# Kernel tuning notes

Measured on AMD Instinct MI355X. Metric: run time of the kernel, lower is better.

The kernel has to match this reference:

```python
import jax, jax.numpy as jnp
import numpy as np

B, H, W, C = 64, 56, 56, 128
WIN, SHIFT, NH = 7, 3, 4
HD = C // NH
N = WIN * WIN
nWh, nWw = H // WIN, W // WIN
nW = nWh * nWw
MLP_H = 4 * C


def _rel_pos_index():
    # same construction as WindowAttention.__init__
    coords = np.stack(np.meshgrid(np.arange(WIN), np.arange(WIN), indexing='ij')).reshape(2, -1)
    rel = coords[:, :, None] - coords[:, None, :]
    rel = rel.transpose(1, 2, 0).copy()
    rel[..., 0] += WIN - 1
    rel[..., 1] += WIN - 1
    rel[..., 0] *= 2 * WIN - 1
    return rel.sum(-1)  # (N, N) int


def _attn_mask():
    # standard SW-MSA mask (0 / -100 like the torch reference)
    img = np.zeros((H, W))
    cnt = 0
    for hs in (slice(0, -WIN), slice(-WIN, -SHIFT), slice(-SHIFT, None)):
        for ws in (slice(0, -WIN), slice(-WIN, -SHIFT), slice(-SHIFT, None)):
            img[hs, ws] = cnt
            cnt += 1
    m = img.reshape(nWh, WIN, nWw, WIN).transpose(0, 2, 1, 3).reshape(nW, N)
    diff = m[:, None, :] - m[:, :, None]
    return np.where(diff != 0, -100.0, 0.0).astype(np.float32)  # (nW, N, N)


def _ln(x, g, b):
    mu = x.mean(-1, keepdims=True)
    var = ((x - mu) ** 2).mean(-1, keepdims=True)
    return (x - mu) / jnp.sqrt(var + 1e-5) * g + b


def setup_inputs() -> dict:
    key = jax.random.key(0)
    ks = jax.random.split(key, 6)
    s = 0.02
    return {
        'x': jax.random.normal(ks[0], (B, H * W, C), jnp.float32),
        'ln1_g': jnp.ones((C,), jnp.float32),
        'ln1_b': jnp.zeros((C,), jnp.float32),
        'qkv_w': jax.random.normal(ks[1], (3 * C, C), jnp.float32) * s,
        'qkv_b': jnp.zeros((3 * C,), jnp.float32),
        'rpb_table': jax.random.normal(ks[2], ((2 * WIN - 1) ** 2, NH), jnp.float32) * s,
        'proj_w': jax.random.normal(ks[3], (C, C), jnp.float32) * s,
        'proj_b': jnp.zeros((C,), jnp.float32),
        'ln2_g': jnp.ones((C,), jnp.float32),
        'ln2_b': jnp.zeros((C,), jnp.float32),
        'fc1_w': jax.random.normal(ks[4], (MLP_H, C), jnp.float32) * s,
        'fc1_b': jnp.zeros((MLP_H,), jnp.float32),
        'fc2_w': jax.random.normal(ks[5], (C, MLP_H), jnp.float32) * s,
        'fc2_b': jnp.zeros((C,), jnp.float32),
    }


def reference(x, ln1_g, ln1_b, qkv_w, qkv_b, rpb_table, proj_w, proj_b,
              ln2_g, ln2_b, fc1_w, fc1_b, fc2_w, fc2_b):
    rpi = jnp.asarray(_rel_pos_index())          # (N, N)
    mask = jnp.asarray(_attn_mask())             # (nW, N, N)

    shortcut = x
    h = _ln(x, ln1_g, ln1_b).reshape(B, H, W, C)
    # cyclic shift
    h = jnp.roll(h, (-SHIFT, -SHIFT), axis=(1, 2))
    # window partition -> (B*nW, N, C)
    wins = h.reshape(B, nWh, WIN, nWw, WIN, C).transpose(0, 1, 3, 2, 4, 5).reshape(B * nW, N, C)

    # window attention
    qkv = (wins @ qkv_w.T + qkv_b).reshape(B * nW, N, 3, NH, HD).transpose(2, 0, 3, 1, 4)
    q, k, v = qkv[0] * (HD ** -0.5), qkv[1], qkv[2]   # (B*nW, NH, N, HD)
    attn = jnp.einsum('bhnd,bhmd->bhnm', q, k)
    bias = rpb_table[rpi.reshape(-1)].reshape(N, N, NH).transpose(2, 0, 1)  # (NH, N, N)
    attn = attn + bias[None]
    attn = attn.reshape(B, nW, NH, N, N) + mask[None, :, None]
    attn = jax.nn.softmax(attn.reshape(B * nW, NH, N, N), axis=-1)
    o = jnp.einsum('bhnm,bhmd->bhnd', attn, v).transpose(0, 2, 1, 3).reshape(B * nW, N, C)
    o = o @ proj_w.T + proj_b

    # window reverse + reverse shift
    o = o.reshape(B, nWh, nWw, WIN, WIN, C).transpose(0, 1, 3, 2, 4, 5).reshape(B, H, W, C)
    o = jnp.roll(o, (SHIFT, SHIFT), axis=(1, 2)).reshape(B, H * W, C)

    x = shortcut + o
    # MLP residual (exact GELU, as nn.GELU default)
    h2 = _ln(x, ln2_g, ln2_b)
    h2 = jax.nn.gelu(h2 @ fc1_w.T + fc1_b, approximate=False) @ fc2_w.T + fc2_b
    return x + h2
```

## Files before the change

kernel.cpp:

```cpp
#include <hip/hip_runtime.h>
#include <math.h>

#define B_  64
#define Cc  128
#define L_  3136

typedef __bf16 b8v __attribute__((ext_vector_type(8)));
typedef __bf16 b4v __attribute__((ext_vector_type(4)));
typedef float  f4v __attribute__((ext_vector_type(4)));

__device__ __forceinline__ f4v mfma16(b8v a, b8v b, f4v c) {
    return __builtin_amdgcn_mfma_f32_16x16x32_bf16(a, b, c, 0, 0, 0);
}
__device__ __forceinline__ int region(int h, int w) {
    int a = (h < 49) ? 0 : ((h < 53) ? 1 : 2);
    int b = (w < 49) ? 0 : ((w < 53) ? 1 : 2);
    return a * 3 + b;
}

__global__ __launch_bounds__(256) void prep_kernel(
    const float* __restrict__ qkv_w, const float* __restrict__ proj_w,
    const float* __restrict__ fc1_w, const float* __restrict__ fc2_w,
    const float* __restrict__ rpb,
    __bf16* __restrict__ wsb, float* __restrict__ bm)
{
    int i = blockIdx.x * 256 + threadIdx.x;
    if      (i <  49152) wsb[i] = (__bf16)qkv_w[i];
    else if (i <  65536) wsb[i] = (__bf16)proj_w[i - 49152];
    else if (i < 131072) wsb[i] = (__bf16)fc1_w[i - 65536];
    else if (i < 196608) wsb[i] = (__bf16)fc2_w[i - 131072];
    else {
        int idx = i - 196608;
        int jj = idx & 63, ii = (idx >> 6) & 63, h = (idx >> 12) & 3, wt = idx >> 14;
        float v;
        if (jj >= 49)      v = -1e30f;
        else if (ii >= 49) v = 0.f;
        else {
            int ih = ii / 7, iw = ii - ih * 7, jh = jj / 7, jw = jj - jh * 7;
            v = rpb[((ih - jh + 6) * 13 + (iw - jw + 6)) * 4 + h];
            int WH = (wt & 2) ? 49 : 0, WW = (wt & 1) ? 49 : 0;
            if (region(WH + ih, WW + iw) != region(WH + jh, WW + jw)) v -= 100.f;
        }
        bm[idx] = v;
    }
}

__global__ __launch_bounds__(256, 2) void swin_kernel(
    const float* __restrict__ x,
    const float* __restrict__ g1, const float* __restrict__ b1,
    const float* __restrict__ qkv_b, const float* __restrict__ proj_b,
    const __bf16* __restrict__ wqkv, const __bf16* __restrict__ wproj,
    const float* __restrict__ bm,
    float* __restrict__ out)
{
    __shared__ __bf16 a_s[64 * 136];
    __shared__ __bf16 Q_s[64 * 136];
    __shared__ __bf16 K_s[64 * 136];
    __shared__ __bf16 VT_s[128 * 72];

    const int tid = threadIdx.x, w = tid >> 6, lane = tid & 63;
    const int quad = lane >> 4, r16 = lane & 15;
    const int blk = blockIdx.x, b = blk >> 6, wi = blk & 63;
    const int wh = wi >> 3, ww = wi & 7;
    const int wt = ((wh == 7) ? 2 : 0) | ((ww == 7) ? 1 : 0);
    const float scale = 0.17677669529663687f;

    {
        f4v gg0 = *(const f4v*)(g1 + r16 * 8), gg1 = *(const f4v*)(g1 + r16 * 8 + 4);
        f4v bb0 = *(const f4v*)(b1 + r16 * 8), bb1 = *(const f4v*)(b1 + r16 * 8 + 4);
        #pragma unroll
        for (int it = 0; it < 4; it++) {
            int local = it * 4 + quad;
            int t = w * 16 + local;
            b8v o;
            #pragma unroll
            for (int e = 0; e < 8; e++) o[e] = (__bf16)0.f;
            if (t < 49) {
                int th = t / 7, tw = t - th * 7;
                int sh = wh * 7 + th + 3; if (sh >= 56) sh -= 56;
                int sw = ww * 7 + tw + 3; if (sw >= 56) sw -= 56;
                const float* xp = x + (b * L_ + sh * 56 + sw) * Cc + r16 * 8;
                f4v x0 = *(const f4v*)(xp), x1 = *(const f4v*)(xp + 4);
                float s = 0.f, q = 0.f;
                #pragma unroll
                for (int e = 0; e < 4; e++) {
                    s += x0[e] + x1[e];
                    q += x0[e] * x0[e] + x1[e] * x1[e];
                }
                s += __shfl_xor(s, 1, 64); q += __shfl_xor(q, 1, 64);
                s += __shfl_xor(s, 2, 64); q += __shfl_xor(q, 2, 64);
                s += __shfl_xor(s, 4, 64); q += __shfl_xor(q, 4, 64);
                s += __shfl_xor(s, 8, 64); q += __shfl_xor(q, 8, 64);
                float mu = s * (1.f / 128.f);
                float rs = rsqrtf(q * (1.f / 128.f) - mu * mu + 1e-5f);
                #pragma unroll
                for (int e = 0; e < 4; e++) {
                    o[e]     = (__bf16)((x0[e] - mu) * rs * gg0[e] + bb0[e]);
                    o[4 + e] = (__bf16)((x1[e] - mu) * rs * gg1[e] + bb1[e]);
                }
            }
            *(b8v*)(a_s + local * 136 + w * 16 * 136 + r16 * 8) = o;
        }
    }
    __syncthreads();

    {
        b8v A[4][4];
        #pragma unroll
        for (int mt = 0; mt < 4; mt++)
            #pragma unroll
            for (int i = 0; i < 4; i++)
                A[mt][i] = *(const b8v*)(a_s + (mt * 16 + r16) * 136 + i * 32 + quad * 8);

        #pragma unroll
        for (int nt6 = 0; nt6 < 6; nt6++) {
            const int col = w * 96 + nt6 * 16;
            const __bf16* bp = wqkv + (col + r16) * 128 + quad * 8;
            b8v B0 = *(const b8v*)(bp),      B1 = *(const b8v*)(bp + 32);
            b8v B2 = *(const b8v*)(bp + 64), B3 = *(const b8v*)(bp + 96);
            float bias = qkv_b[col + r16];
            #pragma unroll
            for (int mt = 0; mt < 4; mt++) {
                f4v acc = {0.f, 0.f, 0.f, 0.f};
                acc = mfma16(A[mt][0], B0, acc);
                acc = mfma16(A[mt][1], B1, acc);
                acc = mfma16(A[mt][2], B2, acc);
                acc = mfma16(A[mt][3], B3, acc);
                if (col < 128) {
                    #pragma unroll
                    for (int r = 0; r < 4; r++)
                        Q_s[(mt * 16 + quad * 4 + r) * 136 + col + r16] =
                            (__bf16)((acc[r] + bias) * scale);
                } else if (col < 256) {
                    #pragma unroll
                    for (int r = 0; r < 4; r++)
                        K_s[(mt * 16 + quad * 4 + r) * 136 + col - 128 + r16] =
                            (__bf16)(acc[r] + bias);
                } else {
                    b4v pk;
                    #pragma unroll
                    for (int r = 0; r < 4; r++) pk[r] = (__bf16)(acc[r] + bias);
                    *(b4v*)(VT_s + (col - 256 + r16) * 72 + mt * 16 + quad * 4) = pk;
                }
            }
        }
    }
    __syncthreads();

    f4v o_acc[4][2];
    #pragma unroll
    for (int h = 0; h < 4; h++)
        #pragma unroll
        for (int n = 0; n < 2; n++)
            o_acc[h][n] = (f4v){0.f, 0.f, 0.f, 0.f};

    const float* bmw = bm + wt * 4 * 4096;
    __bf16* scr = a_s + w * 16 * 136;

    #pragma unroll
    for (int h = 0; h < 4; h++) {
        b8v qf = *(const b8v*)(Q_s + (w * 16 + r16) * 136 + h * 32 + quad * 8);
        f4v s[4];
        #pragma unroll
        for (int nt = 0; nt < 4; nt++) {
            b8v kf = *(const b8v*)(K_s + (nt * 16 + r16) * 136 + h * 32 + quad * 8);
            f4v z = {0.f, 0.f, 0.f, 0.f};
            s[nt] = mfma16(qf, kf, z);
        }
        const float* bmp = bmw + h * 4096 + (w * 16 + quad * 4) * 64 + r16;
        #pragma unroll
        for (int nt = 0; nt < 4; nt++)
            #pragma unroll
            for (int r = 0; r < 4; r++)
                s[nt][r] += bmp[r * 64 + nt * 16];
        {
            float mx[4], sm[4];
            #pragma unroll
            for (int r = 0; r < 4; r++)
                mx[r] = fmaxf(fmaxf(s[0][r], s[1][r]), fmaxf(s[2][r], s[3][r]));
            #pragma unroll
            for (int mk = 1; mk < 16; mk <<= 1)
                #pragma unroll
                for (int r = 0; r < 4; r++)
                    mx[r] = fmaxf(mx[r], __shfl_xor(mx[r], mk, 64));
            #pragma unroll
            for (int r = 0; r < 4; r++) {
                s[0][r] = expf(s[0][r] - mx[r]);
                s[1][r] = expf(s[1][r] - mx[r]);
                s[2][r] = expf(s[2][r] - mx[r]);
                s[3][r] = expf(s[3][r] - mx[r]);
                sm[r] = s[0][r] + s[1][r] + s[2][r] + s[3][r];
            }
            #pragma unroll
            for (int mk = 1; mk < 16; mk <<= 1)
                #pragma unroll
                for (int r = 0; r < 4; r++)
                    sm[r] += __shfl_xor(sm[r], mk, 64);
            #pragma unroll
            for (int r = 0; r < 4; r++) {
                float inv = 1.f / sm[r];
                s[0][r] *= inv; s[1][r] *= inv; s[2][r] *= inv; s[3][r] *= inv;
            }
        }
        #pragma unroll
        for (int nt = 0; nt < 4; nt++)
            #pragma unroll
            for (int r = 0; r < 4; r++)
                scr[(quad * 4 + r) * 136 + nt * 16 + r16] = (__bf16)s[nt][r];
        #pragma unroll
        for (int ks = 0; ks < 2; ks++) {
            b8v pf = *(const b8v*)(scr + r16 * 136 + ks * 32 + quad * 8);
            #pragma unroll
            for (int nt = 0; nt < 2; nt++) {
                b8v vf = *(const b8v*)(VT_s + (h * 32 + nt * 16 + r16) * 72 + ks * 32 + quad * 8);
                o_acc[h][nt] = mfma16(pf, vf, o_acc[h][nt]);
            }
        }
    }

    #pragma unroll
    for (int h = 0; h < 4; h++)
        #pragma unroll
        for (int nt = 0; nt < 2; nt++)
            #pragma unroll
            for (int r = 0; r < 4; r++)
                scr[(quad * 4 + r) * 136 + h * 32 + nt * 16 + r16] = (__bf16)o_acc[h][nt][r];
    __syncthreads();

    {
        b8v O[4][4];
        #pragma unroll
        for (int mt = 0; mt < 4; mt++)
            #pragma unroll
            for (int i = 0; i < 4; i++)
                O[mt][i] = *(const b8v*)(a_s + (mt * 16 + r16) * 136 + i * 32 + quad * 8);

        #pragma unroll
        for (int nt = 0; nt < 2; nt++) {
            const int col = w * 32 + nt * 16;
            const __bf16* bp = wproj + (col + r16) * 128 + quad * 8;
            b8v B0 = *(const b8v*)(bp),      B1 = *(const b8v*)(bp + 32);
            b8v B2 = *(const b8v*)(bp + 64), B3 = *(const b8v*)(bp + 96);
            float pb = proj_b[col + r16];
            #pragma unroll
            for (int mt = 0; mt < 4; mt++) {
                f4v acc = {0.f, 0.f, 0.f, 0.f};
                acc = mfma16(O[mt][0], B0, acc);
                acc = mfma16(O[mt][1], B1, acc);
                acc = mfma16(O[mt][2], B2, acc);
                acc = mfma16(O[mt][3], B3, acc);
                #pragma unroll
                for (int r = 0; r < 4; r++) {
                    int t = mt * 16 + quad * 4 + r;
                    if (t < 49) {
                        int th = t / 7, tw = t - th * 7;
                        int sh = wh * 7 + th + 3; if (sh >= 56) sh -= 56;
                        int sw = ww * 7 + tw + 3; if (sw >= 56) sw -= 56;
                        int off = (b * L_ + sh * 56 + sw) * Cc + col + r16;
                        out[off] = x[off] + acc[r] + pb;
                    }
                }
            }
        }
    }
}

__global__ __launch_bounds__(256, 2) void mlp_kernel(
    float* __restrict__ out,
    const float* __restrict__ g2, const float* __restrict__ b2,
    const __bf16* __restrict__ wfc1, const __bf16* __restrict__ wfc2,
    const float* __restrict__ fc1_b, const float* __restrict__ fc2_b)
{
    __shared__ __align__(16) char u_s[69632];
    __bf16* x2 = (__bf16*)u_s;
    __bf16* h1 = (__bf16*)(u_s + 34816);
    float*  o_s = (float*)u_s;

    const int tid = threadIdx.x, w = tid >> 6, lane = tid & 63;
    const int quad = lane >> 4, r16 = lane & 15;
    const int rowbase = blockIdx.x * 128;

    #pragma unroll
    for (int p = 0; p < 2; p++) {
        const int r = p * 64 + (tid >> 2), sub = tid & 3;
        const float* xp = out + (rowbase + r) * Cc + sub * 32;
        f4v xa[8];
        #pragma unroll
        for (int j = 0; j < 8; j++) xa[j] = *(const f4v*)(xp + j * 4);
        float s = 0.f, q = 0.f;
        #pragma unroll
        for (int j = 0; j < 8; j++)
            #pragma unroll
            for (int e = 0; e < 4; e++) { float v = xa[j][e]; s += v; q += v * v; }
        s += __shfl_xor(s, 1, 64); q += __shfl_xor(q, 1, 64);
        s += __shfl_xor(s, 2, 64); q += __shfl_xor(q, 2, 64);
        float mu = s * (1.f / 128.f);
        float rs = rsqrtf(q * (1.f / 128.f) - mu * mu + 1e-5f);
        #pragma unroll
        for (int j = 0; j < 8; j += 2) {
            int c = sub * 32 + j * 4;
            f4v gg0 = *(const f4v*)(g2 + c), gg1 = *(const f4v*)(g2 + c + 4);
            f4v bb0 = *(const f4v*)(b2 + c), bb1 = *(const f4v*)(b2 + c + 4);
            b8v o;
            #pragma unroll
            for (int e = 0; e < 4; e++) {
                o[e]     = (__bf16)((xa[j][e]     - mu) * rs * gg0[e] + bb0[e]);
                o[4 + e] = (__bf16)((xa[j + 1][e] - mu) * rs * gg1[e] + bb1[e]);
            }
            *(b8v*)(x2 + r * 136 + c) = o;
        }
    }
    __syncthreads();

    f4v acc[8][2];
    #pragma unroll
    for (int mt = 0; mt < 8; mt++)
        #pragma unroll
        for (int nt = 0; nt < 2; nt++)
            acc[mt][nt] = (f4v){0.f, 0.f, 0.f, 0.f};

    for (int hc = 0; hc < 4; hc++) {
        {
            b8v Bf[2][4]; float bias[2];
            #pragma unroll
            for (int nt = 0; nt < 2; nt++) {
                const int col = hc * 128 + w * 32 + nt * 16;
                const __bf16* bp = wfc1 + (col + r16) * 128 + quad * 8;
                Bf[nt][0] = *(const b8v*)(bp);      Bf[nt][1] = *(const b8v*)(bp + 32);
                Bf[nt][2] = *(const b8v*)(bp + 64); Bf[nt][3] = *(const b8v*)(bp + 96);
                bias[nt] = fc1_b[col + r16];
            }
            #pragma unroll 2
            for (int mt = 0; mt < 8; mt++) {
                const __bf16* ap = x2 + (mt * 16 + r16) * 136 + quad * 8;
                b8v A0 = *(const b8v*)(ap),      A1 = *(const b8v*)(ap + 32);
                b8v A2 = *(const b8v*)(ap + 64), A3 = *(const b8v*)(ap + 96);
                f4v a0 = {0.f, 0.f, 0.f, 0.f}, a1 = {0.f, 0.f, 0.f, 0.f};
                a0 = mfma16(A0, Bf[0][0], a0); a1 = mfma16(A0, Bf[1][0], a1);
                a0 = mfma16(A1, Bf[0][1], a0); a1 = mfma16(A1, Bf[1][1], a1);
                a0 = mfma16(A2, Bf[0][2], a0); a1 = mfma16(A2, Bf[1][2], a1);
                a0 = mfma16(A3, Bf[0][3], a0); a1 = mfma16(A3, Bf[1][3], a1);
                #pragma unroll
                for (int r = 0; r < 4; r++) {
                    float v0 = a0[r] + bias[0];
                    float v1 = a1[r] + bias[1];
                    v0 = 0.5f * v0 * (1.f + erff(v0 * 0.70710678118654752f));
                    v1 = 0.5f * v1 * (1.f + erff(v1 * 0.70710678118654752f));
                    h1[(mt * 16 + quad * 4 + r) * 136 + w * 32 + r16]      = (__bf16)v0;
                    h1[(mt * 16 + quad * 4 + r) * 136 + w * 32 + 16 + r16] = (__bf16)v1;
                }
            }
        }
        __syncthreads();
        #pragma unroll
        for (int Ks = 0; Ks < 4; Ks++) {
            b8v Af[8];
            #pragma unroll
            for (int mt = 0; mt < 8; mt++)
                Af[mt] = *(const b8v*)(h1 + (mt * 16 + r16) * 136 + Ks * 32 + quad * 8);
            #pragma unroll
            for (int nt = 0; nt < 2; nt++) {
                const __bf16* bp = wfc2 + (w * 32 + nt * 16 + r16) * 512
                                 + hc * 128 + Ks * 32 + quad * 8;
                b8v Bf = *(const b8v*)(bp);
                #pragma unroll
                for (int mt = 0; mt < 8; mt++)
                    acc[mt][nt] = mfma16(Af[mt], Bf, acc[mt][nt]);
            }
        }
        __syncthreads();
    }

    #pragma unroll
    for (int nt = 0; nt < 2; nt++) {
        const int col = w * 32 + nt * 16 + r16;
        const float fb = fc2_b[col];
        #pragma unroll
        for (int mt = 0; mt < 8; mt++)
            #pragma unroll
            for (int r = 0; r < 4; r++)
                o_s[(mt * 16 + quad * 4 + r) * 132 + col] = acc[mt][nt][r] + fb;
    }
    __syncthreads();

    #pragma unroll
    for (int p = 0; p < 4; p++) {
        const int row = p * 32 + (tid >> 3), colb = (tid & 7) * 16;
        float* op = out + (rowbase + row) * Cc + colb;
        const float* ls = o_s + row * 132 + colb;
        #pragma unroll
        for (int j = 0; j < 4; j++) {
            f4v v = *(const f4v*)(op + j * 4);
            v += *(const f4v*)(ls + j * 4);
            *(f4v*)(op + j * 4) = v;
        }
    }
}

extern "C" void kernel_launch(void* const* d_in, const int* in_sizes, int n_in,
                              void* d_out, int out_size, void* d_ws, size_t ws_size,
                              hipStream_t stream) {
    __bf16* wsb = (__bf16*)d_ws;
    float*  bmp = (float*)((char*)d_ws + 393216);
    prep_kernel<<<1024, 256, 0, stream>>>(
        (const float*)d_in[3], (const float*)d_in[6],
        (const float*)d_in[10], (const float*)d_in[12],
        (const float*)d_in[5], wsb, bmp);
    swin_kernel<<<B_ * 64, 256, 0, stream>>>(
        (const float*)d_in[0],
        (const float*)d_in[1], (const float*)d_in[2],
        (const float*)d_in[4], (const float*)d_in[7],
        wsb, wsb + 49152,
        bmp, (float*)d_out);
    mlp_kernel<<<(B_ * L_) / 128, 256, 0, stream>>>(
        (float*)d_out,
        (const float*)d_in[8], (const float*)d_in[9],
        wsb + 65536, wsb + 131072,
        (const float*)d_in[11], (const float*)d_in[13]);
}
```

Measured before the change: 498.8 us.

## Transpose MFMA outputs for vector stores, shrink LDS, and drop softmax max pass

```diff
diff --git a/kernel.cpp b/kernel.cpp
--- a/kernel.cpp
+++ b/kernel.cpp
@@ -45,7 +45,7 @@
     }
 }
 
-__global__ __launch_bounds__(256, 2) void swin_kernel(
+__global__ __launch_bounds__(256, 3) void swin_kernel(
     const float* __restrict__ x,
     const float* __restrict__ g1, const float* __restrict__ b1,
     const float* __restrict__ qkv_b, const float* __restrict__ proj_b,
@@ -54,7 +54,6 @@
     float* __restrict__ out)
 {
     __shared__ __bf16 a_s[64 * 136];
-    __shared__ __bf16 Q_s[64 * 136];
     __shared__ __bf16 K_s[64 * 136];
     __shared__ __bf16 VT_s[128 * 72];
 
@@ -99,26 +98,47 @@
                     o[4 + e] = (__bf16)((x1[e] - mu) * rs * gg1[e] + bb1[e]);
                 }
             }
-            *(b8v*)(a_s + local * 136 + w * 16 * 136 + r16 * 8) = o;
+            *(b8v*)(a_s + (w * 16 + local) * 136 + r16 * 8) = o;
         }
     }
     __syncthreads();
 
-    {
-        b8v A[4][4];
-        #pragma unroll
-        for (int mt = 0; mt < 4; mt++)
-            #pragma unroll
-            for (int i = 0; i < 4; i++)
-                A[mt][i] = *(const b8v*)(a_s + (mt * 16 + r16) * 136 + i * 32 + quad * 8);
-
-        #pragma unroll
-        for (int nt6 = 0; nt6 < 6; nt6++) {
-            const int col = w * 96 + nt6 * 16;
-            const __bf16* bp = wqkv + (col + r16) * 128 + quad * 8;
-            b8v B0 = *(const b8v*)(bp),      B1 = *(const b8v*)(bp + 32);
-            b8v B2 = *(const b8v*)(bp + 64), B3 = *(const b8v*)(bp + 96);
-            float bias = qkv_b[col + r16];
+    b8v A[4][4];
+    #pragma unroll
+    for (int mt = 0; mt < 4; mt++)
+        #pragma unroll
+        for (int i = 0; i < 4; i++)
+            A[mt][i] = *(const b8v*)(a_s + (mt * 16 + r16) * 136 + i * 32 + quad * 8);
+    __syncthreads();
+
+    #pragma unroll
+    for (int nt6 = 0; nt6 < 6; nt6++) {
+        const int col = w * 96 + nt6 * 16;
+        const __bf16* bp = wqkv + (col + r16) * 128 + quad * 8;
+        b8v B0 = *(const b8v*)(bp),      B1 = *(const b8v*)(bp + 32);
+        b8v B2 = *(const b8v*)(bp + 64), B3 = *(const b8v*)(bp + 96);
+        if (col < 256) {
+            f4v qb = *(const f4v*)(qkv_b + col + quad * 4);
+            #pragma unroll
+            for (int mt = 0; mt < 4; mt++) {
+                f4v acc = {0.f, 0.f, 0.f, 0.f};
+                acc = mfma16(B0, A[mt][0], acc);
+                acc = mfma16(B1, A[mt][1], acc);
+                acc = mfma16(B2, A[mt][2], acc);
+                acc = mfma16(B3, A[mt][3], acc);
+                b4v pk;
+                if (col < 128) {
+                    #pragma unroll
+                    for (int r = 0; r < 4; r++) pk[r] = (__bf16)((acc[r] + qb[r]) * scale);
+                    *(b4v*)(a_s + (mt * 16 + r16) * 136 + col + quad * 4) = pk;
+                } else {
+                    #pragma unroll
+                    for (int r = 0; r < 4; r++) pk[r] = (__bf16)(acc[r] + qb[r]);
+                    *(b4v*)(K_s + (mt * 16 + r16) * 136 + (col - 128) + quad * 4) = pk;
+                }
+            }
+        } else {
+            float vb = qkv_b[col + r16];
             #pragma unroll
             for (int mt = 0; mt < 4; mt++) {
                 f4v acc = {0.f, 0.f, 0.f, 0.f};
@@ -126,26 +146,22 @@
                 acc = mfma16(A[mt][1], B1, acc);
                 acc = mfma16(A[mt][2], B2, acc);
                 acc = mfma16(A[mt][3], B3, acc);
-                if (col < 128) {
-                    #pragma unroll
-                    for (int r = 0; r < 4; r++)
-                        Q_s[(mt * 16 + quad * 4 + r) * 136 + col + r16] =
-                            (__bf16)((acc[r] + bias) * scale);
-                } else if (col < 256) {
-                    #pragma unroll
-                    for (int r = 0; r < 4; r++)
-                        K_s[(mt * 16 + quad * 4 + r) * 136 + col - 128 + r16] =
-                            (__bf16)(acc[r] + bias);
-                } else {
-                    b4v pk;
-                    #pragma unroll
-                    for (int r = 0; r < 4; r++) pk[r] = (__bf16)(acc[r] + bias);
-                    *(b4v*)(VT_s + (col - 256 + r16) * 72 + mt * 16 + quad * 4) = pk;
-                }
+                b4v pk;
+                #pragma unroll
+                for (int r = 0; r < 4; r++) pk[r] = (__bf16)(acc[r] + vb);
+                *(b4v*)(VT_s + (col - 256 + r16) * 72 + mt * 16 + quad * 4) = pk;
             }
         }
     }
     __syncthreads();
+
+    b8v qf[4];
+    #pragma unroll
+    for (int h = 0; h < 4; h++)
+        qf[h] = *(const b8v*)(a_s + (w * 16 + r16) * 136 + h * 32 + quad * 8);
+
+    __bf16* scr = a_s + (w * 16) * 136;
+    const float* bmq = bm + wt * 4 * 4096 + (w * 16 + r16) * 64;
 
     f4v o_acc[4][2];
     #pragma unroll
@@ -154,66 +170,42 @@
         for (int n = 0; n < 2; n++)
             o_acc[h][n] = (f4v){0.f, 0.f, 0.f, 0.f};
 
-    const float* bmw = bm + wt * 4 * 4096;
-    __bf16* scr = a_s + w * 16 * 136;
-
     #pragma unroll
     for (int h = 0; h < 4; h++) {
-        b8v qf = *(const b8v*)(Q_s + (w * 16 + r16) * 136 + h * 32 + quad * 8);
         f4v s[4];
         #pragma unroll
         for (int nt = 0; nt < 4; nt++) {
             b8v kf = *(const b8v*)(K_s + (nt * 16 + r16) * 136 + h * 32 + quad * 8);
             f4v z = {0.f, 0.f, 0.f, 0.f};
-            s[nt] = mfma16(qf, kf, z);
-        }
-        const float* bmp = bmw + h * 4096 + (w * 16 + quad * 4) * 64 + r16;
-        #pragma unroll
-        for (int nt = 0; nt < 4; nt++)
-            #pragma unroll
-            for (int r = 0; r < 4; r++)
-                s[nt][r] += bmp[r * 64 + nt * 16];
-        {
-            float mx[4], sm[4];
-            #pragma unroll
-            for (int r = 0; r < 4; r++)
-                mx[r] = fmaxf(fmaxf(s[0][r], s[1][r]), fmaxf(s[2][r], s[3][r]));
-            #pragma unroll
-            for (int mk = 1; mk < 16; mk <<= 1)
-                #pragma unroll
-                for (int r = 0; r < 4; r++)
-                    mx[r] = fmaxf(mx[r], __shfl_xor(mx[r], mk, 64));
+            s[nt] = mfma16(kf, qf[h], z);
+        }
+        float sm = 0.f;
+        #pragma unroll
+        for (int nt = 0; nt < 4; nt++) {
+            f4v mb = *(const f4v*)(bmq + h * 4096 + nt * 16 + quad * 4);
             #pragma unroll
             for (int r = 0; r < 4; r++) {
-                s[0][r] = expf(s[0][r] - mx[r]);
-                s[1][r] = expf(s[1][r] - mx[r]);
-                s[2][r] = expf(s[2][r] - mx[r]);
-                s[3][r] = expf(s[3][r] - mx[r]);
-                sm[r] = s[0][r] + s[1][r] + s[2][r] + s[3][r];
-            }
-            #pragma unroll
-            for (int mk = 1; mk < 16; mk <<= 1)
-                #pragma unroll
-                for (int r = 0; r < 4; r++)
-                    sm[r] += __shfl_xor(sm[r], mk, 64);
-            #pragma unroll
-            for (int r = 0; r < 4; r++) {
-                float inv = 1.f / sm[r];
-                s[0][r] *= inv; s[1][r] *= inv; s[2][r] *= inv; s[3][r] *= inv;
-            }
-        }
-        #pragma unroll
-        for (int nt = 0; nt < 4; nt++)
-            #pragma unroll
-            for (int r = 0; r < 4; r++)
-                scr[(quad * 4 + r) * 136 + nt * 16 + r16] = (__bf16)s[nt][r];
+                s[nt][r] = __expf(s[nt][r] + mb[r]);
+                sm += s[nt][r];
+            }
+        }
+        sm += __shfl_xor(sm, 16, 64);
+        sm += __shfl_xor(sm, 32, 64);
+        float inv = 1.f / sm;
+        #pragma unroll
+        for (int nt = 0; nt < 4; nt++) {
+            b4v pk;
+            #pragma unroll
+            for (int r = 0; r < 4; r++) pk[r] = (__bf16)(s[nt][r] * inv);
+            *(b4v*)(scr + r16 * 136 + nt * 16 + quad * 4) = pk;
+        }
         #pragma unroll
         for (int ks = 0; ks < 2; ks++) {
             b8v pf = *(const b8v*)(scr + r16 * 136 + ks * 32 + quad * 8);
             #pragma unroll
             for (int nt = 0; nt < 2; nt++) {
                 b8v vf = *(const b8v*)(VT_s + (h * 32 + nt * 16 + r16) * 72 + ks * 32 + quad * 8);
-                o_acc[h][nt] = mfma16(pf, vf, o_acc[h][nt]);
+                o_acc[h][nt] = mfma16(vf, pf, o_acc[h][nt]);
             }
         }
     }
@@ -221,10 +213,12 @@
     #pragma unroll
     for (int h = 0; h < 4; h++)
         #pragma unroll
-        for (int nt = 0; nt < 2; nt++)
-            #pragma unroll
-            for (int r = 0; r < 4; r++)
-                scr[(quad * 4 + r) * 136 + h * 32 + nt * 16 + r16] = (__bf16)o_acc[h][nt][r];
+        for (int nt = 0; nt < 2; nt++) {
+            b4v pk;
+            #pragma unroll
+            for (int r = 0; r < 4; r++) pk[r] = (__bf16)o_acc[h][nt][r];
+            *(b4v*)(scr + r16 * 136 + h * 32 + nt * 16 + quad * 4) = pk;
+        }
     __syncthreads();
 
     {
@@ -241,48 +235,46 @@
             const __bf16* bp = wproj + (col + r16) * 128 + quad * 8;
             b8v B0 = *(const b8v*)(bp),      B1 = *(const b8v*)(bp + 32);
             b8v B2 = *(const b8v*)(bp + 64), B3 = *(const b8v*)(bp + 96);
-            float pb = proj_b[col + r16];
+            f4v pb = *(const f4v*)(proj_b + col + quad * 4);
             #pragma unroll
             for (int mt = 0; mt < 4; mt++) {
                 f4v acc = {0.f, 0.f, 0.f, 0.f};
-                acc = mfma16(O[mt][0], B0, acc);
-                acc = mfma16(O[mt][1], B1, acc);
-                acc = mfma16(O[mt][2], B2, acc);
-                acc = mfma16(O[mt][3], B3, acc);
-                #pragma unroll
-                for (int r = 0; r < 4; r++) {
-                    int t = mt * 16 + quad * 4 + r;
-                    if (t < 49) {
-                        int th = t / 7, tw = t - th * 7;
-                        int sh = wh * 7 + th + 3; if (sh >= 56) sh -= 56;
-                        int sw = ww * 7 + tw + 3; if (sw >= 56) sw -= 56;
-                        int off = (b * L_ + sh * 56 + sw) * Cc + col + r16;
-                        out[off] = x[off] + acc[r] + pb;
-                    }
+                acc = mfma16(B0, O[mt][0], acc);
+                acc = mfma16(B1, O[mt][1], acc);
+                acc = mfma16(B2, O[mt][2], acc);
+                acc = mfma16(B3, O[mt][3], acc);
+                int t = mt * 16 + r16;
+                if (t < 49) {
+                    int th = t / 7, tw = t - th * 7;
+                    int sh = wh * 7 + th + 3; if (sh >= 56) sh -= 56;
+                    int sw = ww * 7 + tw + 3; if (sw >= 56) sw -= 56;
+                    int off = (b * L_ + sh * 56 + sw) * Cc + col + quad * 4;
+                    f4v xr = *(const f4v*)(x + off);
+                    f4v res;
+                    #pragma unroll
+                    for (int r = 0; r < 4; r++) res[r] = xr[r] + acc[r] + pb[r];
+                    *(f4v*)(out + off) = res;
                 }
             }
         }
     }
 }
 
-__global__ __launch_bounds__(256, 2) void mlp_kernel(
+__global__ __launch_bounds__(256, 4) void mlp_kernel(
     float* __restrict__ out,
     const float* __restrict__ g2, const float* __restrict__ b2,
     const __bf16* __restrict__ wfc1, const __bf16* __restrict__ wfc2,
     const float* __restrict__ fc1_b, const float* __restrict__ fc2_b)
 {
-    __shared__ __align__(16) char u_s[69632];
-    __bf16* x2 = (__bf16*)u_s;
-    __bf16* h1 = (__bf16*)(u_s + 34816);
-    float*  o_s = (float*)u_s;
+    __shared__ __bf16 x2[64 * 136];
+    __shared__ __bf16 h1[64 * 136];
 
     const int tid = threadIdx.x, w = tid >> 6, lane = tid & 63;
     const int quad = lane >> 4, r16 = lane & 15;
-    const int rowbase = blockIdx.x * 128;
-
-    #pragma unroll
-    for (int p = 0; p < 2; p++) {
-        const int r = p * 64 + (tid >> 2), sub = tid & 3;
+    const int rowbase = blockIdx.x * 64;
+
+    {
+        const int r = tid >> 2, sub = tid & 3;
         const float* xp = out + (rowbase + r) * Cc + sub * 32;
         f4v xa[8];
         #pragma unroll
@@ -312,51 +304,53 @@
     }
     __syncthreads();
 
-    f4v acc[8][2];
-    #pragma unroll
-    for (int mt = 0; mt < 8; mt++)
+    f4v acc[4][2];
+    #pragma unroll
+    for (int mt = 0; mt < 4; mt++)
         #pragma unroll
         for (int nt = 0; nt < 2; nt++)
             acc[mt][nt] = (f4v){0.f, 0.f, 0.f, 0.f};
 
     for (int hc = 0; hc < 4; hc++) {
         {
-            b8v Bf[2][4]; float bias[2];
+            b8v Bf[2][4]; f4v b14[2];
             #pragma unroll
             for (int nt = 0; nt < 2; nt++) {
                 const int col = hc * 128 + w * 32 + nt * 16;
                 const __bf16* bp = wfc1 + (col + r16) * 128 + quad * 8;
                 Bf[nt][0] = *(const b8v*)(bp);      Bf[nt][1] = *(const b8v*)(bp + 32);
                 Bf[nt][2] = *(const b8v*)(bp + 64); Bf[nt][3] = *(const b8v*)(bp + 96);
-                bias[nt] = fc1_b[col + r16];
-            }
-            #pragma unroll 2
-            for (int mt = 0; mt < 8; mt++) {
+                b14[nt] = *(const f4v*)(fc1_b + col + quad * 4);
+            }
+            #pragma unroll
+            for (int mt = 0; mt < 4; mt++) {
                 const __bf16* ap = x2 + (mt * 16 + r16) * 136 + quad * 8;
                 b8v A0 = *(const b8v*)(ap),      A1 = *(const b8v*)(ap + 32);
                 b8v A2 = *(const b8v*)(ap + 64), A3 = *(const b8v*)(ap + 96);
-                f4v a0 = {0.f, 0.f, 0.f, 0.f}, a1 = {0.f, 0.f, 0.f, 0.f};
-                a0 = mfma16(A0, Bf[0][0], a0); a1 = mfma16(A0, Bf[1][0], a1);
-                a0 = mfma16(A1, Bf[0][1], a0); a1 = mfma16(A1, Bf[1][1], a1);
-                a0 = mfma16(A2, Bf[0][2], a0); a1 = mfma16(A2, Bf[1][2], a1);
-                a0 = mfma16(A3, Bf[0][3], a0); a1 = mfma16(A3, Bf[1][3], a1);
                 #pragma unroll
-                for (int r = 0; r < 4; r++) {
-                    float v0 = a0[r] + bias[0];
-                    float v1 = a1[r] + bias[1];
-                    v0 = 0.5f * v0 * (1.f + erff(v0 * 0.70710678118654752f));
-                    v1 = 0.5f * v1 * (1.f + erff(v1 * 0.70710678118654752f));
-                    h1[(mt * 16 + quad * 4 + r) * 136 + w * 32 + r16]      = (__bf16)v0;
-                    h1[(mt * 16 + quad * 4 + r) * 136 + w * 32 + 16 + r16] = (__bf16)v1;
+                for (int nt = 0; nt < 2; nt++) {
+                    f4v a = {0.f, 0.f, 0.f, 0.f};
+                    a = mfma16(Bf[nt][0], A0, a);
+                    a = mfma16(Bf[nt][1], A1, a);
+                    a = mfma16(Bf[nt][2], A2, a);
+                    a = mfma16(Bf[nt][3], A3, a);
+                    b4v pk;
+                    #pragma unroll
+                    for (int r = 0; r < 4; r++) {
+                        float v = a[r] + b14[nt][r];
+                        v = 0.5f * v * (1.f + erff(v * 0.70710678118654752f));
+                        pk[r] = (__bf16)v;
+                    }
+                    *(b4v*)(h1 + (mt * 16 + r16) * 136 + w * 32 + nt * 16 + quad * 4) = pk;
                 }
             }
         }
         __syncthreads();
         #pragma unroll
         for (int Ks = 0; Ks < 4; Ks++) {
-            b8v Af[8];
-            #pragma unroll
-            for (int mt = 0; mt < 8; mt++)
+            b8v Af[4];
+            #pragma unroll
+            for (int mt = 0; mt < 4; mt++)
                 Af[mt] = *(const b8v*)(h1 + (mt * 16 + r16) * 136 + Ks * 32 + quad * 8);
             #pragma unroll
             for (int nt = 0; nt < 2; nt++) {
@@ -364,35 +358,24 @@
                                  + hc * 128 + Ks * 32 + quad * 8;
                 b8v Bf = *(const b8v*)(bp);
                 #pragma unroll
-                for (int mt = 0; mt < 8; mt++)
-                    acc[mt][nt] = mfma16(Af[mt], Bf, acc[mt][nt]);
-            }
-        }
-        __syncthreads();
+                for (int mt = 0; mt < 4; mt++)
+                    acc[mt][nt] = mfma16(Bf, Af[mt], acc[mt][nt]);
+            }
+        }
+        if (hc < 3) __syncthreads();
     }
 
     #pragma unroll
     for (int nt = 0; nt < 2; nt++) {
-        const int col = w * 32 + nt * 16 + r16;
-        const float fb = fc2_b[col];
-        #pragma unroll
-        for (int mt = 0; mt < 8; mt++)
-            #pragma unroll
-            for (int r = 0; r < 4; r++)
-                o_s[(mt * 16 + quad * 4 + r) * 132 + col] = acc[mt][nt][r] + fb;
-    }
-    __syncthreads();
-
-    #pragma unroll
-    for (int p = 0; p < 4; p++) {
-        const int row = p * 32 + (tid >> 3), colb = (tid & 7) * 16;
-        float* op = out + (rowbase + row) * Cc + colb;
-        const float* ls = o_s + row * 132 + colb;
-        #pragma unroll
-        for (int j = 0; j < 4; j++) {
-            f4v v = *(const f4v*)(op + j * 4);
-            v += *(const f4v*)(ls + j * 4);
-            *(f4v*)(op + j * 4) = v;
+        const int col = w * 32 + nt * 16 + quad * 4;
+        f4v fb = *(const f4v*)(fc2_b + col);
+        #pragma unroll
+        for (int mt = 0; mt < 4; mt++) {
+            float* op = out + (rowbase + mt * 16 + r16) * Cc + col;
+            f4v v = *(const f4v*)op;
+            #pragma unroll
+            for (int r = 0; r < 4; r++) v[r] += acc[mt][nt][r] + fb[r];
+            *(f4v*)op = v;
         }
     }
 }
@@ -412,7 +395,7 @@
         (const float*)d_in[4], (const float*)d_in[7],
         wsb, wsb + 49152,
         bmp, (float*)d_out);
-    mlp_kernel<<<(B_ * L_) / 128, 256, 0, stream>>>(
+    mlp_kernel<<<(B_ * L_) / 64, 256, 0, stream>>>(
         (float*)d_out,
         (const float*)d_in[8], (const float*)d_in[9],
         wsb + 65536, wsb + 131072,
```

Result: faster. 467.0 us (-6.4%).
